# Optimization experiments

Measured on AMD Instinct MI355X. Metric: run time of the kernel, lower is better.

Reference implementation:

```python
import jax, jax.numpy as jnp
import numpy as np

B, N1, N2, C1, C2 = 8, 8192, 2048, 128, 256
O1, O2 = 256, 256
IN_CH = C2 + C1  # 384
BN_EPS = 1e-5


def setup_inputs() -> dict:
    key = jax.random.key(0)
    ks = jax.random.split(key, 6)
    return {
        "xyz1": jax.random.normal(ks[0], (B, N1, 3), dtype=jnp.float32),
        "xyz2": jax.random.normal(ks[1], (B, N2, 3), dtype=jnp.float32),
        "feats1": jax.random.normal(ks[2], (B, C1, N1), dtype=jnp.float32),
        "feats2": jax.random.normal(ks[3], (B, C2, N2), dtype=jnp.float32),
        "W1": jax.random.normal(ks[4], (O1, IN_CH), dtype=jnp.float32) * 0.02,
        "b1": jnp.zeros((O1,), jnp.float32),
        "g1": jnp.ones((O1,), jnp.float32),
        "be1": jnp.zeros((O1,), jnp.float32),
        "W2": jax.random.normal(ks[5], (O2, O1), dtype=jnp.float32) * 0.02,
        "b2": jnp.zeros((O2,), jnp.float32),
        "g2": jnp.ones((O2,), jnp.float32),
        "be2": jnp.zeros((O2,), jnp.float32),
    }


def _bn(x, g, b):
    # eval-mode BatchNorm1d with init running stats (mean=0, var=1)
    return g[None, :, None] * x * (1.0 / jnp.sqrt(1.0 + BN_EPS)) + b[None, :, None]


def reference(xyz1, xyz2, feats1, feats2, W1, b1, g1, be1, W2, b2, g2, be2):
    # pairwise Euclidean distances (B, N1, N2), torch.cdist equivalent
    d2 = (jnp.sum(xyz1 * xyz1, -1)[:, :, None]
          + jnp.sum(xyz2 * xyz2, -1)[:, None, :]
          - 2.0 * jnp.einsum('bnc,bmc->bnm', xyz1, xyz2))
    d = jnp.sqrt(jnp.maximum(d2, 0.0))
    # 3 nearest neighbors (smallest distances)
    neg_d, idx = jax.lax.top_k(-d, 3)          # idx: (B, N1, 3)
    knn_d = jnp.maximum(-neg_d, 1e-8)
    w = 1.0 / knn_d
    w = w / jnp.sum(w, -1, keepdims=True)       # (B, N1, 3)
    # gather neighbor features: feats2 (B,C2,N2) -> (B,N2,C2) -> (B,N1,3,C2)
    f2p = jnp.swapaxes(feats2, 1, 2)
    neigh = f2p[jnp.arange(B)[:, None, None], idx]
    out = jnp.einsum('bnk,bnkc->bcn', w, neigh)  # (B, C2, N1)
    out = jnp.concatenate([out, feats1], axis=1)  # (B, C2+C1, N1)
    # Conv1d(k=1) + BN + ReLU, twice
    h = jax.nn.relu(_bn(jnp.einsum('oc,bcn->bon', W1, out) + b1[None, :, None], g1, be1))
    h = jax.nn.relu(_bn(jnp.einsum('oc,bcn->bon', W2, h) + b2[None, :, None], g2, be2))
    return h
```

## Files before the change

### kernel.cpp

```cpp
#include <hip/hip_runtime.h>

typedef __attribute__((ext_vector_type(8))) short bf16x8;
typedef __attribute__((ext_vector_type(4))) float f32x4;
typedef __attribute__((ext_vector_type(4))) unsigned short u16x4;

__device__ __forceinline__ unsigned short f2bf(float f) {
  unsigned u = __float_as_uint(f);
  u += 0x7FFFu + ((u >> 16) & 1u);
  return (unsigned short)(u >> 16);
}

__global__ __launch_bounds__(256) void prep(
    const float* __restrict__ f1, const float* __restrict__ f2,
    const float* __restrict__ xyz2,
    const float* __restrict__ W1, const float* __restrict__ W2,
    short* __restrict__ ft1, unsigned short* __restrict__ ft2,
    short* __restrict__ wpk1, short* __restrict__ wpk2,
    float4* __restrict__ xyz2s) {
  __shared__ float tile[64][65];
  const int bid = blockIdx.x, t = threadIdx.x;
  const int tj = t & 63, tr = t >> 6;
  if (bid < 1024) {
    int b = bid & 7, i = bid >> 3;
    int j0 = (i & 31) * 64, c0 = (i >> 5) * 64;
#pragma unroll
    for (int p = 0; p < 16; ++p) {
      int ci = p * 4 + tr;
      tile[ci][tj] = f2[(size_t)(b * 256 + c0 + ci) * 2048 + j0 + tj];
    }
    __syncthreads();
#pragma unroll
    for (int p = 0; p < 16; ++p) {
      int jr = p * 4 + tr;
      ft2[(size_t)(b * 2048 + j0 + jr) * 256 + c0 + tj] = f2bf(tile[tj][jr]);
    }
  } else if (bid < 3072) {
    int i = bid - 1024;
    int b = i & 7, ii = i >> 3;
    int j0 = (ii & 127) * 64, c0 = (ii >> 7) * 64;
#pragma unroll
    for (int p = 0; p < 16; ++p) {
      int ci = p * 4 + tr;
      tile[ci][tj] = f1[(size_t)(b * 128 + c0 + ci) * 8192 + j0 + tj];
    }
    __syncthreads();
#pragma unroll
    for (int p = 0; p < 16; ++p) {
      int jr = p * 4 + tr;
      ft1[((size_t)b * 8192 + j0 + jr) * 128 + c0 + tj] = (short)f2bf(tile[tj][jr]);
    }
  } else {
    int id = (bid - 3072) * 256 + t;
    if (id < 98304) {
      int j = id & 7, lane = (id >> 3) & 63, mt = (id >> 9) & 15, kt = id >> 13;
      int o = mt * 16 + (lane & 15);
      int c = kt * 32 + ((lane >> 4) & 3) * 8 + j;
      wpk1[id] = (short)f2bf(W1[o * 384 + c]);
    } else if (id < 163840) {
      int f = id - 98304;
      int j = f & 7, lane = (f >> 3) & 63, mt = (f >> 9) & 15, kt = f >> 13;
      int o = mt * 16 + (lane & 15);
      int c = kt * 32 + ((lane >> 4) & 3) * 8 + j;
      wpk2[f] = (short)f2bf(W2[o * 256 + c]);
    } else {
      int p = id - 163840;
      int b = p >> 11, j = p & 2047;
      const float* q = xyz2 + (size_t)(b * 2048 + j) * 3;
      float px = q[0], py = q[1], pz = q[2];
      float s2 = __fadd_rn(__fadd_rn(__fmul_rn(px, px), __fmul_rn(py, py)),
                           __fmul_rn(pz, pz));
      xyz2s[b * 2048 + j] = make_float4(px, py, pz, s2);
    }
  }
}

__device__ __forceinline__ void merge44d(double a0, double a1, double a2, double a3,
                                         double c0, double c1, double c2, double c3,
                                         double& o0, double& o1, double& o2, double& o3) {
#define POP(OD)                                                           \
  {                                                                       \
    bool s = a0 < c0;                                                     \
    OD = s ? a0 : c0;                                                     \
    double sa0 = s ? a1 : a0, sa1 = s ? a2 : a1, sa2 = s ? a3 : a2;       \
    double sc0 = s ? c0 : c1, sc1 = s ? c1 : c2, sc2 = s ? c2 : c3;       \
    a3 = s ? 1e300 : a3; c3 = s ? c3 : 1e300;                             \
    a0 = sa0; a1 = sa1; a2 = sa2; c0 = sc0; c1 = sc1; c2 = sc2;           \
  }
  POP(o0) POP(o1) POP(o2) POP(o3)
#undef POP
}

__global__ __launch_bounds__(512, 8) void fused(
    const float* __restrict__ xyz1, const float4* __restrict__ xyz2s,
    const unsigned short* __restrict__ ft2, const short* __restrict__ ft1,
    const short* __restrict__ wpk1, const short* __restrict__ wpk2,
    const float* __restrict__ b1, const float* __restrict__ g1, const float* __restrict__ be1,
    const float* __restrict__ b2, const float* __restrict__ g2, const float* __restrict__ be2,
    float* __restrict__ out) {
  __shared__ __align__(16) char XH[32768];
  __shared__ __align__(16) double T4[1024];
  float* W3s = (float*)((char*)T4 + 6144);
  int*  ID3s = (int*)((char*)T4 + 6912);

  const int t = threadIdx.x, lane = t & 63, wid = t >> 6;
  const int blk = blockIdx.x;
  const int b = blk & 7, n0 = (blk >> 3) * 64;
  const int l15 = lane & 15, l4 = lane >> 4;

  float qx, qy, qz, s1;
  {
    const float* p = xyz1 + ((size_t)b * 8192 + n0 + lane) * 3;
    qx = p[0]; qy = p[1]; qz = p[2];
    s1 = __fadd_rn(__fadd_rn(__fmul_rn(qx, qx), __fmul_rn(qy, qy)), __fmul_rn(qz, qz));
  }

  unsigned k0 = 0xFFFFFFFFu, k1 = 0xFFFFFFFFu, k2 = 0xFFFFFFFFu, k3 = 0xFFFFFFFFu;
  unsigned i0 = 0, i1 = 0, i2 = 0, i3 = 0;
  {
    const int jb = __builtin_amdgcn_readfirstlane(wid * 256);
    const float4* __restrict__ pk = xyz2s + (size_t)b * 2048;
#pragma unroll 4
    for (int jo = 0; jo < 256; ++jo) {
      int j = jb + jo;
      float4 P = pk[j];
      float dot = __fadd_rn(__fadd_rn(__fmul_rn(qx, P.x), __fmul_rn(qy, P.y)),
                            __fmul_rn(qz, P.z));
      float d2 = __fsub_rn(__fadd_rn(s1, P.w), __fadd_rn(dot, dot));
      unsigned K = __float_as_uint(fmaxf(d2, 0.0f));
      bool l0 = K < k0, l1 = K < k1, l2 = K < k2, l3 = K < k3;
      unsigned nk0 = min(k0, K);
      unsigned nk1 = min(max(K, k0), k1);
      unsigned nk2 = min(max(K, k1), k2);
      unsigned nk3 = min(max(K, k2), k3);
      unsigned uj = (unsigned)j;
      unsigned ni0 = l0 ? uj : i0;
      unsigned ni1 = l0 ? i0 : (l1 ? uj : i1);
      unsigned ni2 = l1 ? i1 : (l2 ? uj : i2);
      unsigned ni3 = l2 ? i2 : (l3 ? uj : i3);
      k0 = nk0; k1 = nk1; k2 = nk2; k3 = nk3;
      i0 = ni0; i1 = ni1; i2 = ni2; i3 = ni3;
    }
  }
  double key0 = fma((double)k0, 2048.0, (double)i0);
  double key1 = fma((double)k1, 2048.0, (double)i1);
  double key2 = fma((double)k2, 2048.0, (double)i2);
  double key3 = fma((double)k3, 2048.0, (double)i3);

  if (wid >= 4) {
    int w = wid - 4;
    T4[0 * 256 + w * 64 + lane] = key0; T4[1 * 256 + w * 64 + lane] = key1;
    T4[2 * 256 + w * 64 + lane] = key2; T4[3 * 256 + w * 64 + lane] = key3;
  }
  __syncthreads();
  double m10 = 0, m11 = 0, m12 = 0, m13 = 0;
  if (wid < 4) {
    double p0 = T4[0 * 256 + wid * 64 + lane], p1 = T4[1 * 256 + wid * 64 + lane];
    double p2 = T4[2 * 256 + wid * 64 + lane], p3 = T4[3 * 256 + wid * 64 + lane];
    merge44d(key0, key1, key2, key3, p0, p1, p2, p3, m10, m11, m12, m13);
  }
  __syncthreads();
  if (wid == 2 || wid == 3) {
    int w = wid - 2;
    T4[0 * 128 + w * 64 + lane] = m10; T4[1 * 128 + w * 64 + lane] = m11;
    T4[2 * 128 + w * 64 + lane] = m12; T4[3 * 128 + w * 64 + lane] = m13;
  }
  __syncthreads();
  double m20 = 0, m21 = 0, m22 = 0, m23 = 0;
  if (wid < 2) {
    double p0 = T4[0 * 128 + wid * 64 + lane], p1 = T4[1 * 128 + wid * 64 + lane];
    double p2 = T4[2 * 128 + wid * 64 + lane], p3 = T4[3 * 128 + wid * 64 + lane];
    merge44d(m10, m11, m12, m13, p0, p1, p2, p3, m20, m21, m22, m23);
  }
  __syncthreads();
  if (wid == 1) {
    T4[0 * 64 + lane] = m20; T4[1 * 64 + lane] = m21;
    T4[2 * 64 + lane] = m22; T4[3 * 64 + lane] = m23;
  }
  __syncthreads();
  if (wid == 0) {
    double p0 = T4[0 * 64 + lane], p1 = T4[1 * 64 + lane];
    double p2 = T4[2 * 64 + lane], p3 = T4[3 * 64 + lane];
    double mf[4];
    merge44d(m20, m21, m22, m23, p0, p1, p2, p3, mf[0], mf[1], mf[2], mf[3]);
    float e[4]; int ji[4];
#pragma unroll
    for (int s = 0; s < 4; ++s) {
      double qd = mf[s] * (1.0 / 2048.0);
      double qf = trunc(qd);
      double jd = fma(-qf, 2048.0, mf[s]);
      ji[s] = (int)jd;
      e[s] = __fsqrt_rn(__uint_as_float((unsigned)qf));
    }
#define SW(X, Y)                                                          \
  {                                                                       \
    bool sw = (e[X] > e[Y]) || ((e[X] == e[Y]) && (ji[X] > ji[Y]));       \
    float td = e[X]; int ti = ji[X];                                      \
    e[X] = sw ? e[Y] : e[X]; ji[X] = sw ? ji[Y] : ji[X];                  \
    e[Y] = sw ? td : e[Y];   ji[Y] = sw ? ti : ji[Y];                     \
  }
    SW(0, 1) SW(1, 2) SW(2, 3) SW(0, 1) SW(1, 2) SW(0, 1)
#undef SW
    float c0 = fmaxf(e[0], 1e-8f), c1 = fmaxf(e[1], 1e-8f), c2 = fmaxf(e[2], 1e-8f);
    float u0 = 1.0f / c0, u1 = 1.0f / c1, u2 = 1.0f / c2;
    float ss = __fadd_rn(__fadd_rn(u0, u1), u2);
    W3s[lane * 3 + 0] = u0 / ss; W3s[lane * 3 + 1] = u1 / ss; W3s[lane * 3 + 2] = u2 / ss;
    ID3s[lane * 3 + 0] = ji[0]; ID3s[lane * 3 + 1] = ji[1]; ID3s[lane * 3 + 2] = ji[2];
  }
  __syncthreads();

  {
    const int c = t & 255, half = t >> 8;
    const size_t f2b = (size_t)b * 2048 * 256;
#pragma unroll 2
    for (int qi = 0; qi < 32; ++qi) {
      int q = half * 32 + qi;
      int j0 = ID3s[q * 3 + 0], j1 = ID3s[q * 3 + 1], j2 = ID3s[q * 3 + 2];
      float W0 = W3s[q * 3 + 0], W1v = W3s[q * 3 + 1], W2v = W3s[q * 3 + 2];
      float v0 = __uint_as_float((unsigned)ft2[f2b + (size_t)j0 * 256 + c] << 16);
      float v1 = __uint_as_float((unsigned)ft2[f2b + (size_t)j1 * 256 + c] << 16);
      float v2 = __uint_as_float((unsigned)ft2[f2b + (size_t)j2 * 256 + c] << 16);
      float v = W0 * v0 + W1v * v1 + W2v * v2;
      int addr = (q * 512 + c * 2) ^ ((q & 7) << 4);
      *(unsigned short*)(XH + addr) = f2bf(v);
    }
  }
  __syncthreads();

  f32x4 acc[2][4];
#pragma unroll
  for (int m = 0; m < 2; ++m)
#pragma unroll
    for (int n = 0; n < 4; ++n) acc[m][n] = (f32x4){0.f, 0.f, 0.f, 0.f};

#pragma unroll
  for (int kt = 0; kt < 8; ++kt) {
    bf16x8 a[2], bb[4];
#pragma unroll
    for (int m = 0; m < 2; ++m)
      a[m] = *(const bf16x8*)(wpk1 + ((size_t)(kt * 16 + wid * 2 + m) * 64 + lane) * 8);
#pragma unroll
    for (int nt = 0; nt < 4; ++nt) {
      int q = nt * 16 + l15;
      int addr = q * 512 + ((kt * 64 + l4 * 16) ^ ((q & 7) << 4));
      bb[nt] = *(const bf16x8*)(XH + addr);
    }
#pragma unroll
    for (int m = 0; m < 2; ++m)
#pragma unroll
      for (int nt = 0; nt < 4; ++nt)
        acc[m][nt] = __builtin_amdgcn_mfma_f32_16x16x32_bf16(a[m], bb[nt], acc[m][nt], 0, 0, 0);
  }
#pragma unroll
  for (int kt = 8; kt < 12; ++kt) {
    bf16x8 a[2], bb[4];
#pragma unroll
    for (int m = 0; m < 2; ++m)
      a[m] = *(const bf16x8*)(wpk1 + ((size_t)(kt * 16 + wid * 2 + m) * 64 + lane) * 8);
#pragma unroll
    for (int nt = 0; nt < 4; ++nt)
      bb[nt] = *(const bf16x8*)(ft1 + ((size_t)b * 8192 + n0 + nt * 16 + l15) * 128 +
                                (kt - 8) * 32 + l4 * 8);
#pragma unroll
    for (int m = 0; m < 2; ++m)
#pragma unroll
      for (int nt = 0; nt < 4; ++nt)
        acc[m][nt] = __builtin_amdgcn_mfma_f32_16x16x32_bf16(a[m], bb[nt], acc[m][nt], 0, 0, 0);
  }
  __syncthreads();

  const float BNINV = 0.99999500003749972f;
#pragma unroll
  for (int m = 0; m < 2; ++m) {
    int cb = wid * 32 + m * 16 + l4 * 4;
    float gv[4], bv[4], ev[4];
#pragma unroll
    for (int r = 0; r < 4; ++r) {
      gv[r] = g1[cb + r] * BNINV; bv[r] = b1[cb + r]; ev[r] = be1[cb + r];
    }
#pragma unroll
    for (int nt = 0; nt < 4; ++nt) {
      int q = nt * 16 + l15;
      u16x4 pk4;
#pragma unroll
      for (int r = 0; r < 4; ++r)
        pk4[r] = f2bf(fmaxf((acc[m][nt][r] + bv[r]) * gv[r] + ev[r], 0.0f));
      *(u16x4*)(XH + ((q * 512 + cb * 2) ^ ((q & 7) << 4))) = pk4;
    }
  }
  __syncthreads();

#pragma unroll
  for (int m = 0; m < 2; ++m)
#pragma unroll
    for (int n = 0; n < 4; ++n) acc[m][n] = (f32x4){0.f, 0.f, 0.f, 0.f};
#pragma unroll
  for (int kt = 0; kt < 8; ++kt) {
    bf16x8 a[2], bb[4];
#pragma unroll
    for (int m = 0; m < 2; ++m)
      a[m] = *(const bf16x8*)(wpk2 + ((size_t)(kt * 16 + wid * 2 + m) * 64 + lane) * 8);
#pragma unroll
    for (int nt = 0; nt < 4; ++nt) {
      int q = nt * 16 + l15;
      int addr = q * 512 + ((kt * 64 + l4 * 16) ^ ((q & 7) << 4));
      bb[nt] = *(const bf16x8*)(XH + addr);
    }
#pragma unroll
    for (int m = 0; m < 2; ++m)
#pragma unroll
      for (int nt = 0; nt < 4; ++nt)
        acc[m][nt] = __builtin_amdgcn_mfma_f32_16x16x32_bf16(a[m], bb[nt], acc[m][nt], 0, 0, 0);
  }

#pragma unroll
  for (int m = 0; m < 2; ++m) {
    int ob = wid * 32 + m * 16 + l4 * 4;
    float gv[4], bv[4], ev[4];
#pragma unroll
    for (int r = 0; r < 4; ++r) {
      gv[r] = g2[ob + r] * BNINV; bv[r] = b2[ob + r]; ev[r] = be2[ob + r];
    }
#pragma unroll
    for (int nt = 0; nt < 4; ++nt) {
      int nn = n0 + nt * 16 + l15;
#pragma unroll
      for (int r = 0; r < 4; ++r)
        out[((size_t)b * 256 + ob + r) * 8192 + nn] =
            fmaxf((acc[m][nt][r] + bv[r]) * gv[r] + ev[r], 0.0f);
    }
  }
}

extern "C" void kernel_launch(void* const* d_in, const int* in_sizes, int n_in,
                              void* d_out, int out_size, void* d_ws, size_t ws_size,
                              hipStream_t stream) {
  (void)in_sizes; (void)n_in; (void)out_size; (void)ws_size;
  const float* xyz1   = (const float*)d_in[0];
  const float* xyz2   = (const float*)d_in[1];
  const float* feats1 = (const float*)d_in[2];
  const float* feats2 = (const float*)d_in[3];
  const float* W1  = (const float*)d_in[4];
  const float* b1  = (const float*)d_in[5];
  const float* g1  = (const float*)d_in[6];
  const float* be1 = (const float*)d_in[7];
  const float* W2  = (const float*)d_in[8];
  const float* b2  = (const float*)d_in[9];
  const float* g2  = (const float*)d_in[10];
  const float* be2 = (const float*)d_in[11];
  float* out = (float*)d_out;

  char* ws = (char*)d_ws;
  short*          wpk1  = (short*)(ws);
  short*          wpk2  = (short*)(ws + 196608);
  float4*         xyz2s = (float4*)(ws + 327680);
  unsigned short* ft2   = (unsigned short*)(ws + 589824);
  short*          ft1   = (short*)(ws + 8978432);

  prep<<<3776, 256, 0, stream>>>(feats1, feats2, xyz2, W1, W2,
                                 ft1, ft2, wpk1, wpk2, xyz2s);
  fused<<<1024, 512, 0, stream>>>(xyz1, xyz2s, ft2, ft1, wpk1, wpk2,
                                  b1, g1, be1, b2, g2, be2, out);
}
```

Baseline: 267.0 us.

## Stage xyz2 in LDS, vectorize prep transposes, relax fused launch bounds

The fused kernel now cooperatively copies the batch's 2048 xyz2 points into shared memory (XH) before the KNN scan. The scan then reads them from LDS instead of issuing scalar/uniform global loads per iteration. The prep transposes switch to float4 loads and 4-wide bf16 stores. The min-waves hint is dropped from fused's launch bounds, which frees the register budget but may lower occupancy. The extra barrier and LDS traffic are the cost, and XH must not be in use elsewhere at that point.

```diff
diff --git a/kernel.cpp b/kernel.cpp
--- a/kernel.cpp
+++ b/kernel.cpp
@@ -19,35 +19,46 @@
     float4* __restrict__ xyz2s) {
   __shared__ float tile[64][65];
   const int bid = blockIdx.x, t = threadIdx.x;
-  const int tj = t & 63, tr = t >> 6;
   if (bid < 1024) {
     int b = bid & 7, i = bid >> 3;
     int j0 = (i & 31) * 64, c0 = (i >> 5) * 64;
-#pragma unroll
-    for (int p = 0; p < 16; ++p) {
-      int ci = p * 4 + tr;
-      tile[ci][tj] = f2[(size_t)(b * 256 + c0 + ci) * 2048 + j0 + tj];
+    int r = t >> 4, c4 = (t & 15) * 4;
+#pragma unroll
+    for (int p = 0; p < 4; ++p) {
+      int ci = p * 16 + r;
+      float4 v = *(const float4*)&f2[(size_t)(b * 256 + c0 + ci) * 2048 + j0 + c4];
+      tile[ci][c4] = v.x; tile[ci][c4 + 1] = v.y;
+      tile[ci][c4 + 2] = v.z; tile[ci][c4 + 3] = v.w;
     }
     __syncthreads();
 #pragma unroll
-    for (int p = 0; p < 16; ++p) {
-      int jr = p * 4 + tr;
-      ft2[(size_t)(b * 2048 + j0 + jr) * 256 + c0 + tj] = f2bf(tile[tj][jr]);
+    for (int p = 0; p < 4; ++p) {
+      int jr = p * 16 + r;
+      u16x4 o;
+#pragma unroll
+      for (int k = 0; k < 4; ++k) o[k] = f2bf(tile[c4 + k][jr]);
+      *(u16x4*)&ft2[(size_t)(b * 2048 + j0 + jr) * 256 + c0 + c4] = o;
     }
   } else if (bid < 3072) {
     int i = bid - 1024;
     int b = i & 7, ii = i >> 3;
     int j0 = (ii & 127) * 64, c0 = (ii >> 7) * 64;
-#pragma unroll
-    for (int p = 0; p < 16; ++p) {
-      int ci = p * 4 + tr;
-      tile[ci][tj] = f1[(size_t)(b * 128 + c0 + ci) * 8192 + j0 + tj];
+    int r = t >> 4, c4 = (t & 15) * 4;
+#pragma unroll
+    for (int p = 0; p < 4; ++p) {
+      int ci = p * 16 + r;
+      float4 v = *(const float4*)&f1[(size_t)(b * 128 + c0 + ci) * 8192 + j0 + c4];
+      tile[ci][c4] = v.x; tile[ci][c4 + 1] = v.y;
+      tile[ci][c4 + 2] = v.z; tile[ci][c4 + 3] = v.w;
     }
     __syncthreads();
 #pragma unroll
-    for (int p = 0; p < 16; ++p) {
-      int jr = p * 4 + tr;
-      ft1[((size_t)b * 8192 + j0 + jr) * 128 + c0 + tj] = (short)f2bf(tile[tj][jr]);
+    for (int p = 0; p < 4; ++p) {
+      int jr = p * 16 + r;
+      u16x4 o;
+#pragma unroll
+      for (int k = 0; k < 4; ++k) o[k] = f2bf(tile[c4 + k][jr]);
+      *(u16x4*)&ft1[((size_t)b * 8192 + j0 + jr) * 128 + c0 + c4] = o;
     }
   } else {
     int id = (bid - 3072) * 256 + t;
@@ -90,7 +101,7 @@
 #undef POP
 }
 
-__global__ __launch_bounds__(512, 8) void fused(
+__global__ __launch_bounds__(512) void fused(
     const float* __restrict__ xyz1, const float4* __restrict__ xyz2s,
     const unsigned short* __restrict__ ft2, const short* __restrict__ ft1,
     const short* __restrict__ wpk1, const short* __restrict__ wpk2,
@@ -107,22 +118,27 @@
   const int b = blk & 7, n0 = (blk >> 3) * 64;
   const int l15 = lane & 15, l4 = lane >> 4;
 
+  {
+    float4* pkB = (float4*)XH;
+    for (int j = t; j < 2048; j += 512) pkB[j] = xyz2s[b * 2048 + j];
+  }
   float qx, qy, qz, s1;
   {
     const float* p = xyz1 + ((size_t)b * 8192 + n0 + lane) * 3;
     qx = p[0]; qy = p[1]; qz = p[2];
     s1 = __fadd_rn(__fadd_rn(__fmul_rn(qx, qx), __fmul_rn(qy, qy)), __fmul_rn(qz, qz));
   }
+  __syncthreads();
 
   unsigned k0 = 0xFFFFFFFFu, k1 = 0xFFFFFFFFu, k2 = 0xFFFFFFFFu, k3 = 0xFFFFFFFFu;
   unsigned i0 = 0, i1 = 0, i2 = 0, i3 = 0;
   {
-    const int jb = __builtin_amdgcn_readfirstlane(wid * 256);
-    const float4* __restrict__ pk = xyz2s + (size_t)b * 2048;
+    const float4* __restrict__ pkB = (const float4*)XH;
+    const int jb = wid * 256;
 #pragma unroll 4
     for (int jo = 0; jo < 256; ++jo) {
       int j = jb + jo;
-      float4 P = pk[j];
+      float4 P = pkB[j];
       float dot = __fadd_rn(__fadd_rn(__fmul_rn(qx, P.x), __fmul_rn(qy, P.y)),
                             __fmul_rn(qz, P.z));
       float d2 = __fsub_rn(__fadd_rn(s1, P.w), __fadd_rn(dot, dot));
```

New measurement: 249.7 us. 1.07x faster.
